# Performance work log

Measured on AMD Instinct MI355X. Metric: run time of the kernel, lower is better.

The kernel has to match this reference:

```python
import jax, jax.numpy as jnp
import numpy as np

N_HEAD = 16
LN_EPS = 1e-5     # torch LayerNorm default
ATTN_EPS = 1e-6   # fast-transformers CausalLinearAttention eps


def layer_norm(x, g, b):
    mu = x.mean(-1, keepdims=True)
    var = ((x - mu) ** 2).mean(-1, keepdims=True)
    return (x - mu) * jax.lax.rsqrt(var + LN_EPS) * g + b


def favor(x, omega):
    # Favor/Performer softmax-kernel features.
    # x: [B,S,H,dh], omega: [dh, m/2] -> phi: [B,S,H,m] with m = 2*(dh//2) = dh
    dh = x.shape[-1]
    m = 2 * omega.shape[-1]
    xs = x * (dh ** -0.25)  # x * sqrt(softmax_temp), softmax_temp = 1/sqrt(dh)
    u = jnp.einsum('bshd,dm->bshm', xs, omega)
    h = 0.5 * jnp.sum(xs * xs, axis=-1, keepdims=True)  # ||x||^2 / 2
    return jnp.concatenate([jnp.exp(u - h), jnp.exp(-u - h)], axis=-1) * (m ** -0.5)


def causal_linear_attention(q, k, v):
    # q,k: [B,S,H,M] feature-mapped; v: [B,S,H,Dv]
    # out[i] = (phiQ_i @ sum_{j<=i} phiK_j v_j^T) / (phiQ_i . sum_{j<=i} phiK_j)
    B, S, H, M = q.shape
    Dv = v.shape[-1]
    qT = jnp.moveaxis(q, 1, 0)  # [S,B,H,M]
    kT = jnp.moveaxis(k, 1, 0)
    vT = jnp.moveaxis(v, 1, 0)  # [S,B,H,Dv]
    S0 = jnp.zeros((B, H, M, Dv), q.dtype)
    z0 = jnp.zeros((B, H, M), q.dtype)

    def step(carry, qkv):
        Sst, zst = carry
        qi, ki, vi = qkv
        Sst = Sst + ki[..., :, None] * vi[..., None, :]  # [B,H,M,Dv]
        zst = zst + ki                                   # [B,H,M]
        num = jnp.einsum('bhm,bhmd->bhd', qi, Sst)
        den = jnp.einsum('bhm,bhm->bh', qi, zst) + ATTN_EPS
        return (Sst, zst), num / den[..., None]

    _, out = jax.lax.scan(step, (S0, z0), (qT, kT, vT))
    return jnp.moveaxis(out, 0, 1)  # [B,S,H,Dv]


def forward(x, Wq, bq, Wk, bk, Wv, bv, Wo, bo, omega,
            ln1_g, ln1_b, ln2_g, ln2_b, W1, bf1, W2, bf2):
    L = Wq.shape[0]
    B, S, D = x.shape
    dh = D // N_HEAD
    out = x
    for l in range(L):  # fixed small layer count
        q = (out @ Wq[l] + bq[l]).reshape(B, S, N_HEAD, dh)
        k = (out @ Wk[l] + bk[l]).reshape(B, S, N_HEAD, dh)
        v = (out @ Wv[l] + bv[l]).reshape(B, S, N_HEAD, dh)
        Qf = favor(q, omega[l])
        Kf = favor(k, omega[l])
        a = causal_linear_attention(Qf, Kf, v).reshape(B, S, D)
        a = a @ Wo[l] + bo[l]
        h = layer_norm(out + a, ln1_g[l], ln1_b[l])          # norm1 (post-norm)
        y = jax.nn.relu(h @ W1[l] + bf1[l]) @ W2[l] + bf2[l]  # FFN
        out = layer_norm(h + y, ln2_g[l], ln2_b[l])          # norm2
    return out


def setup_inputs() -> dict:
    key = jax.random.key(0)
    L, B, S, D, DFF = 3, 2, 1024, 1024, 4096
    dh = D // N_HEAD
    ks = jax.random.split(key, 8)
    g = lambda k, shape: jax.random.normal(k, shape, jnp.float32) * 0.02
    return {
        'x': jax.random.normal(ks[0], (B, S, D), jnp.float32),
        'Wq': g(ks[1], (L, D, D)), 'bq': jnp.zeros((L, D), jnp.float32),
        'Wk': g(ks[2], (L, D, D)), 'bk': jnp.zeros((L, D), jnp.float32),
        'Wv': g(ks[3], (L, D, D)), 'bv': jnp.zeros((L, D), jnp.float32),
        'Wo': g(ks[4], (L, D, D)), 'bo': jnp.zeros((L, D), jnp.float32),
        'omega': jax.random.normal(ks[5], (L, dh, dh // 2), jnp.float32),
        'ln1_g': jnp.ones((L, D), jnp.float32), 'ln1_b': jnp.zeros((L, D), jnp.float32),
        'ln2_g': jnp.ones((L, D), jnp.float32), 'ln2_b': jnp.zeros((L, D), jnp.float32),
        'W1': g(ks[6], (L, D, DFF)), 'bf1': jnp.zeros((L, DFF), jnp.float32),
        'W2': g(ks[7], (L, DFF, D)), 'bf2': jnp.zeros((L, D), jnp.float32),
    }


def reference(x, Wq, bq, Wk, bk, Wv, bv, Wo, bo, omega,
              ln1_g, ln1_b, ln2_g, ln2_b, W1, bf1, W2, bf2):
    return forward(x, Wq, bq, Wk, bk, Wv, bv, Wo, bo, omega,
                   ln1_g, ln1_b, ln2_g, ln2_b, W1, bf1, W2, bf2)
```

## Files before the change

### kernel.cpp

```cpp
#include <hip/hip_runtime.h>

typedef unsigned int u32;
typedef unsigned short u16;
typedef unsigned long long u64;

#define LN_EPS 1e-5f
#define ATTN_EPS 1e-6f

typedef __bf16 bf16x8 __attribute__((ext_vector_type(8)));
typedef short shortx8 __attribute__((ext_vector_type(8)));
typedef float fx4 __attribute__((ext_vector_type(4)));

__device__ __forceinline__ u16 f2bf(float f){
  union{float f; u32 u;} x; x.f = f;
  u32 r = 0x7fffu + ((x.u>>16)&1u);
  return (u16)((x.u + r)>>16);
}
__device__ __forceinline__ float bf2f(u16 u){
  union{u32 u; float f;} x; x.u = ((u32)u)<<16; return x.f;
}
__device__ __forceinline__ bf16x8 ldfrag(const u16* p){
  return __builtin_bit_cast(bf16x8, *(const shortx8*)p);
}

__device__ __forceinline__ void async16(const void* g, void* l){
  typedef const __attribute__((address_space(1))) void gas_t;
  typedef __attribute__((address_space(3))) void las_t;
  __builtin_amdgcn_global_load_lds((gas_t*)(u64)g, (las_t*)(u32)(u64)l, 16, 0, 0);
}

__global__ void detect_kernel(const u16* __restrict__ ln1g, int* __restrict__ flag){
  if (threadIdx.x == 0 && blockIdx.x == 0)
    *flag = (ln1g[0] == 0x3F80u) ? 1 : 0;
}

__global__ __launch_bounds__(256) void cvt_small(
    const void* p0, const void* p1, const void* p2, const void* p3,
    const void* p4, const void* p5, const void* p6, const void* p7,
    const void* p8, const void* p9, const void* p10,
    float* __restrict__ out, const int* __restrict__ flagp)
{
  int i = blockIdx.x*256 + threadIdx.x;
  if (i >= 46080) return;
  const void* src; int off;
  if      (i < 3072)  { src=p0;  off=i; }
  else if (i < 6144)  { src=p1;  off=i-3072; }
  else if (i < 9216)  { src=p2;  off=i-6144; }
  else if (i < 12288) { src=p3;  off=i-9216; }
  else if (i < 18432) { src=p4;  off=i-12288; }
  else if (i < 21504) { src=p5;  off=i-18432; }
  else if (i < 24576) { src=p6;  off=i-21504; }
  else if (i < 27648) { src=p7;  off=i-24576; }
  else if (i < 30720) { src=p8;  off=i-27648; }
  else if (i < 43008) { src=p9;  off=i-30720; }
  else                { src=p10; off=i-43008; }
  float v;
  if (*flagp){ union{u32 u; float f;} x; x.u = ((u32)((const u16*)src)[off])<<16; v = x.f; }
  else v = ((const float*)src)[off];
  out[i] = v;
}

__global__ __launch_bounds__(256) void cvt_x(const void* __restrict__ in, float* __restrict__ out,
                                             u16* __restrict__ outbf, int n, const int* __restrict__ flagp){
  int i = blockIdx.x*256 + threadIdx.x;
  if (i >= n) return;
  float v;
  if (*flagp){ union{u32 u; float f;} x; x.u = ((u32)((const u16*)in)[i])<<16; v = x.f; }
  else v = ((const float*)in)[i];
  out[i] = v;
  outbf[i] = f2bf(v);
}

__global__ __launch_bounds__(256) void transpose_cvt(
    const void* __restrict__ W, size_t eoff, u16* __restrict__ Wt,
    int K, int N, const int* __restrict__ flagp)
{
  __shared__ float s[32][33];
  const int bx = blockIdx.x, by = blockIdx.y;
  const int tid = threadIdx.x;
  const int c = tid & 31, r = tid >> 5;
  const int isbf = *flagp;
#pragma unroll
  for (int i = 0; i < 4; ++i){
    int k = by*32 + r + i*8, n = bx*32 + c;
    size_t idx = eoff + (size_t)k*N + n;
    float v;
    if (isbf){ union{u32 u; float f;} x; x.u = ((u32)((const u16*)W)[idx])<<16; v = x.f; }
    else v = ((const float*)W)[idx];
    s[r + i*8][c] = v;
  }
  __syncthreads();
#pragma unroll
  for (int i = 0; i < 4; ++i){
    int n = bx*32 + r + i*8, k = by*32 + c;
    Wt[(size_t)n*K + k] = f2bf(s[c][r + i*8]);
  }
}

__global__ __launch_bounds__(256) void transpose_cvt4(
    const void* __restrict__ W0, const void* __restrict__ W1,
    const void* __restrict__ W2, const void* __restrict__ W3,
    size_t eoff, u16* __restrict__ Wt, size_t wtz,
    int K, int N, const int* __restrict__ flagp)
{
  __shared__ float s[32][33];
  const int z = blockIdx.z;
  const void* W = (z==0)?W0:((z==1)?W1:((z==2)?W2:W3));
  Wt += (size_t)z * wtz;
  const int bx = blockIdx.x, by = blockIdx.y;
  const int tid = threadIdx.x;
  const int c = tid & 31, r = tid >> 5;
  const int isbf = *flagp;
#pragma unroll
  for (int i = 0; i < 4; ++i){
    int k = by*32 + r + i*8, n = bx*32 + c;
    size_t idx = eoff + (size_t)k*N + n;
    float v;
    if (isbf){ union{u32 u; float f;} x; x.u = ((u32)((const u16*)W)[idx])<<16; v = x.f; }
    else v = ((const float*)W)[idx];
    s[r + i*8][c] = v;
  }
  __syncthreads();
#pragma unroll
  for (int i = 0; i < 4; ++i){
    int n = bx*32 + r + i*8, k = by*32 + c;
    Wt[(size_t)n*K + k] = f2bf(s[c][r + i*8]);
  }
}

__global__ __launch_bounds__(512, 1) void mfma_gemm(
    const u16* __restrict__ A, const u16* __restrict__ W,
    const float* __restrict__ bias,
    float* __restrict__ C, u16* __restrict__ Cbf,
    int N, int Kst, int kstep_z, int klen,
    size_t wz, size_t cz, int bz, int bias_all, int relu)
{
  __shared__ u16 As[3][128*32];
  __shared__ u16 Bs[3][128*32];
  const int z = blockIdx.z;
  W    += (size_t)z * wz;
  bias += (size_t)z * bz;
  if (C) C += (size_t)z * cz;
  const int kbeg = z * kstep_z;
  const int tid = threadIdx.x;
  const int lane = tid & 63, wid = tid >> 6;

  int bx = blockIdx.x, by = blockIdx.y;
  {
    const int gx = gridDim.x, gy = gridDim.y;
    if (((gx & 3) == 0) && ((gy & 1) == 0)) {
      const int cw = gx >> 2, ch = gy >> 1;
      if (((cw & (cw-1)) == 0) && ((ch & (ch-1)) == 0)) {
        const int o = by*gx + bx;
        const int xcd = o & 7, k = o >> 3;
        const int lgw = 31 - __clz(cw);
        bx = (xcd & 3)*cw + (k & (cw-1));
        by = (xcd >> 2)*ch + (k >> lgw);
      }
    }
  }
  const int row0 = by * 128, col0 = bx * 128;

  const int ar = tid >> 2, ae = (tid & 3) << 3;
  const u16* gA0 = A + (size_t)(row0 + ar)*Kst + kbeg + ae;
  const u16* gB0 = W + (size_t)(col0 + ar)*Kst + kbeg + ae;

  const int iters = klen >> 5;
#pragma unroll
  for (int s = 0; s < 2; ++s){
    const int ko = s*32;
    async16(gA0 + ko, &As[s][tid*8]);
    async16(gB0 + ko, &Bs[s][tid*8]);
  }

  const int quad = lane >> 4, l16 = lane & 15;
  const int wr = (wid >> 2) * 64, wc = (wid & 3) * 32;
  fx4 acc[4][2] = {};

  for (int it = 0; it < iters; ++it){
    const int cur = it % 3;
    __builtin_amdgcn_s_waitcnt(0x0F72);
    __builtin_amdgcn_s_barrier();
    {
      const int nx   = (it + 2 < iters) ? (it + 2) : (iters - 1);
      const int nbuf = (it + 2) % 3;
      const int ko = nx*32;
      async16(gA0 + ko, &As[nbuf][tid*8]);
      async16(gB0 + ko, &Bs[nbuf][tid*8]);
    }
    bf16x8 af[4], bfr[2];
#pragma unroll
    for (int t = 0; t < 4; ++t)
      af[t] = ldfrag(&As[cur][(wr + t*16 + l16)*32 + quad*8]);
#pragma unroll
    for (int u = 0; u < 2; ++u)
      bfr[u] = ldfrag(&Bs[cur][(wc + u*16 + l16)*32 + quad*8]);
#pragma unroll
    for (int t = 0; t < 4; ++t)
#pragma unroll
      for (int u = 0; u < 2; ++u)
        acc[t][u] = __builtin_amdgcn_mfma_f32_16x16x32_bf16(af[t], bfr[u], acc[t][u], 0, 0, 0);
  }
  __builtin_amdgcn_s_waitcnt(0x0F70);

  const int r0 = quad * 4;
#pragma unroll
  for (int u = 0; u < 2; ++u){
    const int col = col0 + wc + u*16 + l16;
    const float bv = (bias_all || z == 0) ? bias[col] : 0.f;
#pragma unroll
    for (int t = 0; t < 4; ++t){
      const int rowb = row0 + wr + t*16 + r0;
#pragma unroll
      for (int r = 0; r < 4; ++r){
        float v = acc[t][u][r] + bv;
        if (relu) v = fmaxf(v, 0.f);
        if (C)   C[(size_t)(rowb + r)*N + col] = v;
        if (Cbf) Cbf[(size_t)(rowb + r)*N + col] = f2bf(v);
      }
    }
  }
}

__global__ __launch_bounds__(256) void favor_kernel(
    float* __restrict__ Q, float* __restrict__ Kp, const float* __restrict__ omega,
    u16* __restrict__ Qb, u16* __restrict__ Kb)
{
  __shared__ float sh[4][64];
  __shared__ float sho[64][32];
  int tid = threadIdx.x;
  for (int i = tid; i < 2048; i += 256)
    sho[i>>5][i&31] = omega[i];
  int wv = tid >> 6, lane = tid & 63;
  int th = blockIdx.x*4 + wv;
  size_t base = (size_t)(th >> 4) * 1024 + (size_t)(th & 15) * 64;
  int jm = lane & 31;
  float sgn = (lane < 32) ? 1.f : -1.f;
  for (int w = 0; w < 2; ++w){
    float* p = w ? Kp : Q;
    float xs = p[base + lane] * 0.35355339059327373f;
    __syncthreads();
    sh[wv][lane] = xs;
    __syncthreads();
    float u = 0.f, hh = 0.f;
#pragma unroll
    for (int d = 0; d < 64; ++d){
      float xv = sh[wv][d];
      u  = fmaf(xv, sho[d][jm], u);
      hh = fmaf(xv, xv, hh);
    }
    float phi = expf(sgn*u - 0.5f*hh) * 0.125f;
    if (w) p[base + lane] = phi;
    (w ? Kb : Qb)[base + lane] = f2bf(phi);
  }
}

__global__ __launch_bounds__(256) void chunk_kv(
    const float* __restrict__ Kf, const float* __restrict__ V,
    float* __restrict__ KV, float* __restrict__ Ksum)
{
  __shared__ float Ks[64][64];
  __shared__ float Vs[64][64];
  int blk = blockIdx.x;
  int c = blk & 15, h = (blk >> 4) & 15, b = blk >> 8;
  int tid = threadIdx.x;
  for (int i = tid; i < 1024; i += 256){
    int j = i >> 4, m4 = (i & 15) << 2;
    size_t src = ((size_t)(b*1024 + c*64 + j)*16 + h)*64 + m4;
    *(float4*)&Ks[j][m4] = *(const float4*)&Kf[src];
    *(float4*)&Vs[j][m4] = *(const float4*)&V[src];
  }
  __syncthreads();
  int m = tid & 63, dg = tid >> 6;
  float acc[16] = {0.f};
  for (int j = 0; j < 64; ++j){
    float kv = Ks[j][m];
#pragma unroll
    for (int di = 0; di < 16; ++di)
      acc[di] = fmaf(Vs[j][dg*16+di], kv, acc[di]);
  }
  size_t outb = (size_t)blk * 4096;
#pragma unroll
  for (int di = 0; di < 16; ++di)
    KV[outb + (size_t)(dg*16+di)*64 + m] = acc[di];
  if (tid < 64){
    float s = 0.f;
    for (int j = 0; j < 64; ++j) s += Ks[j][tid];
    Ksum[(size_t)blk*64 + tid] = s;
  }
}

__global__ __launch_bounds__(256) void chunk_scan(float* __restrict__ KV, float* __restrict__ Ksum)
{
  int blk = blockIdx.x;
  int bh = blk >> 4, ec = blk & 15;
  int e = ec*256 + threadIdx.x;
  size_t base = (size_t)bh * 65536 + e;
  float run = 0.f;
  for (int c = 0; c < 16; ++c){
    size_t idx = base + (size_t)c*4096;
    float t = KV[idx]; KV[idx] = run; run += t;
  }
  if (ec == 0 && threadIdx.x < 64){
    size_t kb = (size_t)bh * 1024 + threadIdx.x;
    float rz = 0.f;
    for (int c = 0; c < 16; ++c){
      size_t idx = kb + c*64;
      float t = Ksum[idx]; Ksum[idx] = rz; rz += t;
    }
  }
}

__global__ __launch_bounds__(256) void attn_kernel(
    const u16* __restrict__ Qbf, const u16* __restrict__ Kbf,
    const float* __restrict__ V, const float* __restrict__ KVt,
    const float* __restrict__ Ksum, u16* __restrict__ Outbf)
{
  __shared__ u16 Qs[64][72];
  __shared__ u16 Ks[64][72];
  __shared__ u16 Ss[64][72];
  __shared__ u16 Vt[64][72];
  __shared__ u16 Pt[64][72];
  __shared__ float Vrow[64][68];
  __shared__ float densum[64];

  const int blk = blockIdx.x;
  const int c = blk & 15, h = (blk >> 4) & 15, b = blk >> 8;
  const int tid = threadIdx.x;
  const int lane = tid & 63, w = tid >> 6;
  const int quad = lane >> 4, l16 = lane & 15;
  const int t0 = b*1024 + c*64;

  {
    const int r = tid >> 2, q4 = (tid & 3) << 4;
    size_t g = (size_t)(t0 + r)*1024 + h*64 + q4;
    *(uint4*)&Qs[r][q4]   = *(const uint4*)(Qbf + g);
    *(uint4*)&Qs[r][q4+8] = *(const uint4*)(Qbf + g + 8);
    *(uint4*)&Ks[r][q4]   = *(const uint4*)(Kbf + g);
    *(uint4*)&Ks[r][q4+8] = *(const uint4*)(Kbf + g + 8);
    const float* vg = V + g;
    *(float4*)&Vrow[r][q4+0]  = *(const float4*)(vg+0);
    *(float4*)&Vrow[r][q4+4]  = *(const float4*)(vg+4);
    *(float4*)&Vrow[r][q4+8]  = *(const float4*)(vg+8);
    *(float4*)&Vrow[r][q4+12] = *(const float4*)(vg+12);
    const float* pg = KVt + (size_t)blk*4096 + r*64 + q4;
    u16 tmp[16];
#pragma unroll
    for (int j = 0; j < 16; ++j) tmp[j] = f2bf(pg[j]);
    *(uint4*)&Pt[r][q4]   = *(uint4*)&tmp[0];
    *(uint4*)&Pt[r][q4+8] = *(uint4*)&tmp[8];
  }
  __syncthreads();
  {
    const int d = tid >> 2, j16 = (tid & 3) << 4;
    u16 tmp[16];
#pragma unroll
    for (int j = 0; j < 16; ++j) tmp[j] = f2bf(Vrow[j16+j][d]);
    *(uint4*)&Vt[d][j16]   = *(uint4*)&tmp[0];
    *(uint4*)&Vt[d][j16+8] = *(uint4*)&tmp[8];
  }

  const int iw0 = w*16;
  bf16x8 aq0 = ldfrag(&Qs[iw0+l16][quad*8]);
  bf16x8 aq1 = ldfrag(&Qs[iw0+l16][32+quad*8]);
  fx4 sacc[4];
#pragma unroll
  for (int u = 0; u < 4; ++u){
    sacc[u] = (fx4){0.f,0.f,0.f,0.f};
    bf16x8 b0 = ldfrag(&Ks[u*16+l16][quad*8]);
    bf16x8 b1 = ldfrag(&Ks[u*16+l16][32+quad*8]);
    sacc[u] = __builtin_amdgcn_mfma_f32_16x16x32_bf16(aq0, b0, sacc[u], 0, 0, 0);
    sacc[u] = __builtin_amdgcn_mfma_f32_16x16x32_bf16(aq1, b1, sacc[u], 0, 0, 0);
  }
  float rs[4] = {0.f,0.f,0.f,0.f};
#pragma unroll
  for (int u = 0; u < 4; ++u){
    const int jl = u*16 + l16;
#pragma unroll
    for (int r = 0; r < 4; ++r){
      const int il = iw0 + quad*4 + r;
      float v = (jl <= il) ? sacc[u][r] : 0.f;
      rs[r] += v;
      Ss[il][jl] = f2bf(v);
    }
  }
#pragma unroll
  for (int off = 1; off < 16; off <<= 1){
#pragma unroll
    for (int r = 0; r < 4; ++r) rs[r] += __shfl_xor(rs[r], off);
  }
  if (l16 == 0){
#pragma unroll
    for (int r = 0; r < 4; ++r) densum[iw0 + quad*4 + r] = rs[r];
  }
  __syncthreads();

  {
    const int row = iw0 + l16;
    const float* zp = Ksum + (size_t)blk*64;
    float dp = 0.f;
#pragma unroll
    for (int m = 0; m < 16; ++m){
      const int mm = quad*16 + m;
      dp = fmaf(bf2f(Qs[row][mm]), zp[mm], dp);
    }
    dp += __shfl_xor(dp, 16);
    dp += __shfl_xor(dp, 32);
    if (quad == 0) densum[row] = densum[row] + dp + ATTN_EPS;
  }
  __syncthreads();

  bf16x8 as0 = ldfrag(&Ss[iw0+l16][quad*8]);
  bf16x8 as1 = ldfrag(&Ss[iw0+l16][32+quad*8]);
  fx4 oacc[4];
#pragma unroll
  for (int u = 0; u < 4; ++u){
    const int d0 = u*16;
    oacc[u] = (fx4){0.f,0.f,0.f,0.f};
    oacc[u] = __builtin_amdgcn_mfma_f32_16x16x32_bf16(as0, ldfrag(&Vt[d0+l16][quad*8]),    oacc[u], 0,0,0);
    oacc[u] = __builtin_amdgcn_mfma_f32_16x16x32_bf16(as1, ldfrag(&Vt[d0+l16][32+quad*8]), oacc[u], 0,0,0);
    oacc[u] = __builtin_amdgcn_mfma_f32_16x16x32_bf16(aq0, ldfrag(&Pt[d0+l16][quad*8]),    oacc[u], 0,0,0);
    oacc[u] = __builtin_amdgcn_mfma_f32_16x16x32_bf16(aq1, ldfrag(&Pt[d0+l16][32+quad*8]), oacc[u], 0,0,0);
  }
#pragma unroll
  for (int u = 0; u < 4; ++u){
    const int d = u*16 + l16;
#pragma unroll
    for (int r = 0; r < 4; ++r){
      const int il = iw0 + quad*4 + r;
      const float o = oacc[u][r] / densum[il];
      Outbf[(size_t)(t0 + il)*1024 + h*64 + d] = f2bf(o);
    }
  }
}

__global__ __launch_bounds__(256) void resid_ln(
    const float* __restrict__ X, const float* __restrict__ Y0, const float* __restrict__ Y1,
    const float* __restrict__ g, const float* __restrict__ b,
    float* __restrict__ Dst, u16* __restrict__ DstBf,
    void* __restrict__ OutPtr, const int* __restrict__ flagp)
{
  __shared__ float rs[4], rss[4];
  int row = blockIdx.x, tid = threadIdx.x;
  int lane = tid & 63, wv = tid >> 6;
  size_t base = (size_t)row * 1024;
  int c = tid << 2;
  float4 xv = *(const float4*)&X[base + c];
  float4 y0 = *(const float4*)&Y0[base + c];
  float4 y1 = *(const float4*)&Y1[base + c];
  float v0 = xv.x+y0.x+y1.x, v1 = xv.y+y0.y+y1.y, v2 = xv.z+y0.z+y1.z, v3 = xv.w+y0.w+y1.w;
  float s = v0+v1+v2+v3;
  float ss = v0*v0+v1*v1+v2*v2+v3*v3;
  for (int off = 32; off; off >>= 1){
    s  += __shfl_down(s, off);
    ss += __shfl_down(ss, off);
  }
  if (lane == 0){ rs[wv] = s; rss[wv] = ss; }
  __syncthreads();
  float S  = rs[0]+rs[1]+rs[2]+rs[3];
  float SS = rss[0]+rss[1]+rss[2]+rss[3];
  float mu = S * (1.f/1024.f);
  float var = SS * (1.f/1024.f) - mu*mu;
  float rinv = rsqrtf(var + LN_EPS);
  float4 gv = *(const float4*)(g + c);
  float4 bb = *(const float4*)(b + c);
  float o0 = (v0-mu)*rinv*gv.x + bb.x;
  float o1 = (v1-mu)*rinv*gv.y + bb.y;
  float o2 = (v2-mu)*rinv*gv.z + bb.z;
  float o3 = (v3-mu)*rinv*gv.w + bb.w;
  *(float4*)&Dst[base + c] = make_float4(o0,o1,o2,o3);
  uint2 ob;
  ob.x = (u32)f2bf(o0) | ((u32)f2bf(o1) << 16);
  ob.y = (u32)f2bf(o2) | ((u32)f2bf(o3) << 16);
  *(uint2*)(DstBf + base + c) = ob;
  if (OutPtr){
    if (*flagp){
      *(uint2*)((u16*)OutPtr + base + c) = ob;
    } else {
      *(float4*)((float*)OutPtr + base + c) = make_float4(o0,o1,o2,o3);
    }
  }
}

extern "C" void kernel_launch(void* const* d_in, const int* in_sizes, int n_in,
                              void* d_out, int out_size, void* d_ws, size_t ws_size,
                              hipStream_t stream)
{
  (void)in_sizes; (void)n_in; (void)out_size; (void)ws_size;

  float* ws   = (float*)d_ws;
  float* bufA = ws;
  float* bufQ = bufA + 2097152;
  float* bufK = bufQ + 2097152;
  float* bufV = bufK + 2097152;
  float* KV   = bufV + 2097152;
  float* Ks   = KV   + 2097152;
  float* smallP = Ks + 32768;
  float* pend = smallP + 46080;
  int* flag = (int*)pend;
  u16* abf  = (u16*)(pend + 4);
  u16* hbf  = abf  + 2097152;
  u16* t1bf = hbf  + 2097152;
  u16* fbf  = t1bf + 2097152;
  u16* Wt   = fbf  + 8388608;
  u16* qpbf = Wt   + 4194304;
  u16* kpbf = qpbf + 2097152;

  float* bqF  = smallP + 0;
  float* boF  = smallP + 9216;
  float* omF  = smallP + 12288;
  float* l1gF = smallP + 18432;
  float* l1bF = smallP + 21504;
  float* l2gF = smallP + 24576;
  float* l2bF = smallP + 27648;
  float* bf1F = smallP + 30720;
  float* bf2F = smallP + 43008;

  detect_kernel<<<1, 64, 0, stream>>>((const u16*)d_in[10], flag);
  cvt_small<<<180, 256, 0, stream>>>(d_in[2], d_in[4], d_in[6], d_in[8], d_in[9],
                                     d_in[10], d_in[11], d_in[12], d_in[13],
                                     d_in[15], d_in[17], smallP, flag);
  cvt_x<<<8192, 256, 0, stream>>>(d_in[0], bufA, abf, 2097152, flag);

  dim3 tQKVO(32, 32, 4);
  dim3 tF1(128, 32);
  dim3 tF2(32, 128);
  dim3 gQKV(8, 16, 3);
  dim3 gO(8, 16, 2);
  dim3 gF1(32, 16, 1);
  dim3 gF2(8, 16, 2);

  for (int l = 0; l < 3; ++l){
    size_t offD = (size_t)l * 1048576;
    size_t offF = (size_t)l * 4194304;

    transpose_cvt4<<<tQKVO, 256, 0, stream>>>(d_in[1], d_in[3], d_in[5], d_in[7],
                                              offD, Wt, 1048576, 1024, 1024, flag);

    mfma_gemm<<<gQKV, 512, 0, stream>>>(abf, Wt, bqF + l*1024, bufQ, (u16*)nullptr,
                                        1024, 1024, 0, 1024,
                                        1048576, 2097152, 3072, 1, 0);
    favor_kernel<<<8192, 256, 0, stream>>>(bufQ, bufK, omF + l*2048, qpbf, kpbf);
    chunk_kv<<<512, 256, 0, stream>>>(bufK, bufV, KV, Ks);
    chunk_scan<<<512, 256, 0, stream>>>(KV, Ks);
    attn_kernel<<<512, 256, 0, stream>>>(qpbf, kpbf, bufV, KV, Ks, t1bf);

    mfma_gemm<<<gO, 512, 0, stream>>>(t1bf, Wt + 3145728, boF + l*1024, bufQ, (u16*)nullptr,
                                      1024, 1024, 512, 512,
                                      0, 4194304, 0, 0, 0);
    resid_ln<<<2048, 256, 0, stream>>>(bufA, bufQ, bufV, l1gF + l*1024, l1bF + l*1024,
                                       bufK, hbf, nullptr, flag);

    transpose_cvt<<<tF1, 256, 0, stream>>>(d_in[14], offF, Wt, 1024, 4096, flag);
    mfma_gemm<<<gF1, 512, 0, stream>>>(hbf, Wt, bf1F + l*4096, (float*)nullptr, fbf,
                                       4096, 1024, 0, 1024,
                                       0, 0, 0, 1, 1);

    transpose_cvt<<<tF2, 256, 0, stream>>>(d_in[16], offF, Wt, 4096, 1024, flag);
    mfma_gemm<<<gF2, 512, 0, stream>>>(fbf, Wt, bf2F + l*1024, bufQ, (u16*)nullptr,
                                       1024, 4096, 2048, 2048,
                                       0, 4194304, 0, 0, 0);

    resid_ln<<<2048, 256, 0, stream>>>(bufK, bufQ, bufV, l2gF + l*1024, l2bF + l*1024,
                                       bufA, abf, (l == 2) ? d_out : nullptr, flag);
  }
}
```

Measured before the change: 776.9 us.

## Hoist all weight transposes out of layer loop and shrink GEMM tiles

All layers' weights are now transposed and converted to bf16 up front in batched launches, so the per-layer transpose kernels disappear and their launches serialize less. The GEMM kernel moves from 512 threads with 128x128 tiles to 256 threads with 128x64 tiles, which doubles the number of workgroups. FFN2 split-K goes from 2 to 4 partial sums, and resid_ln is extended to add four partials. In exchange the workspace grows substantially to hold every layer's transposed weights, and the extra split-K partial buffers add memory traffic.

```diff
diff --git a/kernel.cpp b/kernel.cpp
--- a/kernel.cpp
+++ b/kernel.cpp
@@ -71,11 +71,13 @@
   outbf[i] = f2bf(v);
 }
 
-__global__ __launch_bounds__(256) void transpose_cvt(
-    const void* __restrict__ W, size_t eoff, u16* __restrict__ Wt,
-    int K, int N, const int* __restrict__ flagp)
+__global__ __launch_bounds__(256) void transpose_cvtL(
+    const void* __restrict__ W, u16* __restrict__ Wt,
+    int K, int N, size_t zsrc, size_t zdst, const int* __restrict__ flagp)
 {
   __shared__ float s[32][33];
+  const size_t eoff = (size_t)blockIdx.z * zsrc;
+  Wt += (size_t)blockIdx.z * zdst;
   const int bx = blockIdx.x, by = blockIdx.y;
   const int tid = threadIdx.x;
   const int c = tid & 31, r = tid >> 5;
@@ -97,16 +99,16 @@
   }
 }
 
-__global__ __launch_bounds__(256) void transpose_cvt4(
+__global__ __launch_bounds__(256) void transpose_cvtQ(
     const void* __restrict__ W0, const void* __restrict__ W1,
     const void* __restrict__ W2, const void* __restrict__ W3,
-    size_t eoff, u16* __restrict__ Wt, size_t wtz,
-    int K, int N, const int* __restrict__ flagp)
+    u16* __restrict__ Wt, const int* __restrict__ flagp)
 {
   __shared__ float s[32][33];
-  const int z = blockIdx.z;
-  const void* W = (z==0)?W0:((z==1)?W1:((z==2)?W2:W3));
-  Wt += (size_t)z * wtz;
+  const int z = blockIdx.z, l = z >> 2, m = z & 3;
+  const void* W = (m==0)?W0:((m==1)?W1:((m==2)?W2:W3));
+  const size_t eoff = (size_t)l * 1048576;
+  Wt += (size_t)z * 1048576;
   const int bx = blockIdx.x, by = blockIdx.y;
   const int tid = threadIdx.x;
   const int c = tid & 31, r = tid >> 5;
@@ -114,7 +116,7 @@
 #pragma unroll
   for (int i = 0; i < 4; ++i){
     int k = by*32 + r + i*8, n = bx*32 + c;
-    size_t idx = eoff + (size_t)k*N + n;
+    size_t idx = eoff + (size_t)k*1024 + n;
     float v;
     if (isbf){ union{u32 u; float f;} x; x.u = ((u32)((const u16*)W)[idx])<<16; v = x.f; }
     else v = ((const float*)W)[idx];
@@ -124,11 +126,11 @@
 #pragma unroll
   for (int i = 0; i < 4; ++i){
     int n = bx*32 + r + i*8, k = by*32 + c;
-    Wt[(size_t)n*K + k] = f2bf(s[c][r + i*8]);
-  }
-}
-
-__global__ __launch_bounds__(512, 1) void mfma_gemm(
+    Wt[(size_t)n*1024 + k] = f2bf(s[c][r + i*8]);
+  }
+}
+
+__global__ __launch_bounds__(256, 1) void mfma_gemm(
     const u16* __restrict__ A, const u16* __restrict__ W,
     const float* __restrict__ bias,
     float* __restrict__ C, u16* __restrict__ Cbf,
@@ -136,7 +138,7 @@
     size_t wz, size_t cz, int bz, int bias_all, int relu)
 {
   __shared__ u16 As[3][128*32];
-  __shared__ u16 Bs[3][128*32];
+  __shared__ u16 Bs[3][64*32];
   const int z = blockIdx.z;
   W    += (size_t)z * wz;
   bias += (size_t)z * bz;
@@ -159,10 +161,11 @@
       }
     }
   }
-  const int row0 = by * 128, col0 = bx * 128;
+  const int row0 = by * 128, col0 = bx * 64;
 
   const int ar = tid >> 2, ae = (tid & 3) << 3;
   const u16* gA0 = A + (size_t)(row0 + ar)*Kst + kbeg + ae;
+  const u16* gA1 = A + (size_t)(row0 + 64 + ar)*Kst + kbeg + ae;
   const u16* gB0 = W + (size_t)(col0 + ar)*Kst + kbeg + ae;
 
   const int iters = klen >> 5;
@@ -170,22 +173,24 @@
   for (int s = 0; s < 2; ++s){
     const int ko = s*32;
     async16(gA0 + ko, &As[s][tid*8]);
+    async16(gA1 + ko, &As[s][2048 + tid*8]);
     async16(gB0 + ko, &Bs[s][tid*8]);
   }
 
   const int quad = lane >> 4, l16 = lane & 15;
-  const int wr = (wid >> 2) * 64, wc = (wid & 3) * 32;
+  const int wr = (wid >> 1) * 64, wc = (wid & 1) * 32;
   fx4 acc[4][2] = {};
 
   for (int it = 0; it < iters; ++it){
     const int cur = it % 3;
-    __builtin_amdgcn_s_waitcnt(0x0F72);
+    __builtin_amdgcn_s_waitcnt(0x0F73);
     __builtin_amdgcn_s_barrier();
     {
       const int nx   = (it + 2 < iters) ? (it + 2) : (iters - 1);
       const int nbuf = (it + 2) % 3;
       const int ko = nx*32;
       async16(gA0 + ko, &As[nbuf][tid*8]);
+      async16(gA1 + ko, &As[nbuf][2048 + tid*8]);
       async16(gB0 + ko, &Bs[nbuf][tid*8]);
     }
     bf16x8 af[4], bfr[2];
@@ -436,6 +441,7 @@
 
 __global__ __launch_bounds__(256) void resid_ln(
     const float* __restrict__ X, const float* __restrict__ Y0, const float* __restrict__ Y1,
+    const float* __restrict__ Y2, const float* __restrict__ Y3,
     const float* __restrict__ g, const float* __restrict__ b,
     float* __restrict__ Dst, u16* __restrict__ DstBf,
     void* __restrict__ OutPtr, const int* __restrict__ flagp)
@@ -449,6 +455,11 @@
   float4 y0 = *(const float4*)&Y0[base + c];
   float4 y1 = *(const float4*)&Y1[base + c];
   float v0 = xv.x+y0.x+y1.x, v1 = xv.y+y0.y+y1.y, v2 = xv.z+y0.z+y1.z, v3 = xv.w+y0.w+y1.w;
+  if (Y2){
+    float4 y2 = *(const float4*)&Y2[base + c];
+    float4 y3 = *(const float4*)&Y3[base + c];
+    v0 += y2.x + y3.x; v1 += y2.y + y3.y; v2 += y2.z + y3.z; v3 += y2.w + y3.w;
+  }
   float s = v0+v1+v2+v3;
   float ss = v0*v0+v1*v1+v2*v2+v3*v3;
   for (int off = 32; off; off >>= 1){
@@ -489,12 +500,13 @@
   (void)in_sizes; (void)n_in; (void)out_size; (void)ws_size;
 
   float* ws   = (float*)d_ws;
-  float* bufA = ws;
-  float* bufQ = bufA + 2097152;
-  float* bufK = bufQ + 2097152;
-  float* bufV = bufK + 2097152;
-  float* KV   = bufV + 2097152;
-  float* Ks   = KV   + 2097152;
+  float* R    = ws;
+  float* P0   = R  + 2097152;
+  float* P1   = P0 + 2097152;
+  float* P2   = P1 + 2097152;
+  float* P3   = P2 + 2097152;
+  float* KVb  = P3 + 2097152;
+  float* Ks   = KVb + 2097152;
   float* smallP = Ks + 32768;
   float* pend = smallP + 46080;
   int* flag = (int*)pend;
@@ -502,9 +514,11 @@
   u16* hbf  = abf  + 2097152;
   u16* t1bf = hbf  + 2097152;
   u16* fbf  = t1bf + 2097152;
-  u16* Wt   = fbf  + 8388608;
-  u16* qpbf = Wt   + 4194304;
+  u16* qpbf = fbf  + 8388608;
   u16* kpbf = qpbf + 2097152;
+  u16* WtQ  = kpbf + 2097152;
+  u16* WtF1 = WtQ  + 12582912;
+  u16* WtF2 = WtF1 + 12582912;
 
   float* bqF  = smallP + 0;
   float* boF  = smallP + 9216;
@@ -520,48 +534,48 @@
   cvt_small<<<180, 256, 0, stream>>>(d_in[2], d_in[4], d_in[6], d_in[8], d_in[9],
                                      d_in[10], d_in[11], d_in[12], d_in[13],
                                      d_in[15], d_in[17], smallP, flag);
-  cvt_x<<<8192, 256, 0, stream>>>(d_in[0], bufA, abf, 2097152, flag);
-
-  dim3 tQKVO(32, 32, 4);
-  dim3 tF1(128, 32);
-  dim3 tF2(32, 128);
-  dim3 gQKV(8, 16, 3);
-  dim3 gO(8, 16, 2);
-  dim3 gF1(32, 16, 1);
-  dim3 gF2(8, 16, 2);
+  cvt_x<<<8192, 256, 0, stream>>>(d_in[0], R, abf, 2097152, flag);
+
+  transpose_cvtQ<<<dim3(32, 32, 12), 256, 0, stream>>>(d_in[1], d_in[3], d_in[5], d_in[7],
+                                                       WtQ, flag);
+  transpose_cvtL<<<dim3(128, 32, 3), 256, 0, stream>>>(d_in[14], WtF1, 1024, 4096,
+                                                       4194304, 4194304, flag);
+  transpose_cvtL<<<dim3(32, 128, 3), 256, 0, stream>>>(d_in[16], WtF2, 4096, 1024,
+                                                       4194304, 4194304, flag);
+
+  dim3 gQKV(16, 16, 3);
+  dim3 gO(16, 16, 2);
+  dim3 gF1(64, 16, 1);
+  dim3 gF2(16, 16, 4);
 
   for (int l = 0; l < 3; ++l){
-    size_t offD = (size_t)l * 1048576;
-    size_t offF = (size_t)l * 4194304;
-
-    transpose_cvt4<<<tQKVO, 256, 0, stream>>>(d_in[1], d_in[3], d_in[5], d_in[7],
-                                              offD, Wt, 1048576, 1024, 1024, flag);
-
-    mfma_gemm<<<gQKV, 512, 0, stream>>>(abf, Wt, bqF + l*1024, bufQ, (u16*)nullptr,
+    const size_t wQ = (size_t)l * 4194304;
+
+    mfma_gemm<<<gQKV, 256, 0, stream>>>(abf, WtQ + wQ, bqF + l*1024, P0, (u16*)nullptr,
                                         1024, 1024, 0, 1024,
                                         1048576, 2097152, 3072, 1, 0);
-    favor_kernel<<<8192, 256, 0, stream>>>(bufQ, bufK, omF + l*2048, qpbf, kpbf);
-    chunk_kv<<<512, 256, 0, stream>>>(bufK, bufV, KV, Ks);
-    chunk_scan<<<512, 256, 0, stream>>>(KV, Ks);
-    attn_kernel<<<512, 256, 0, stream>>>(qpbf, kpbf, bufV, KV, Ks, t1bf);
-
-    mfma_gemm<<<gO, 512, 0, stream>>>(t1bf, Wt + 3145728, boF + l*1024, bufQ, (u16*)nullptr,
+    favor_kernel<<<8192, 256, 0, stream>>>(P0, P1, omF + l*2048, qpbf, kpbf);
+    chunk_kv<<<512, 256, 0, stream>>>(P1, P2, KVb, Ks);
+    chunk_scan<<<512, 256, 0, stream>>>(KVb, Ks);
+    attn_kernel<<<512, 256, 0, stream>>>(qpbf, kpbf, P2, KVb, Ks, t1bf);
+
+    mfma_gemm<<<gO, 256, 0, stream>>>(t1bf, WtQ + wQ + 3145728, boF + l*1024, P0, (u16*)nullptr,
                                       1024, 1024, 512, 512,
-                                      0, 4194304, 0, 0, 0);
-    resid_ln<<<2048, 256, 0, stream>>>(bufA, bufQ, bufV, l1gF + l*1024, l1bF + l*1024,
-                                       bufK, hbf, nullptr, flag);
-
-    transpose_cvt<<<tF1, 256, 0, stream>>>(d_in[14], offF, Wt, 1024, 4096, flag);
-    mfma_gemm<<<gF1, 512, 0, stream>>>(hbf, Wt, bf1F + l*4096, (float*)nullptr, fbf,
+                                      0, 2097152, 0, 0, 0);
+    resid_ln<<<2048, 256, 0, stream>>>(R, P0, P1, nullptr, nullptr,
+                                       l1gF + l*1024, l1bF + l*1024,
+                                       KVb, hbf, nullptr, flag);
+
+    mfma_gemm<<<gF1, 256, 0, stream>>>(hbf, WtF1 + wQ, bf1F + l*4096, (float*)nullptr, fbf,
                                        4096, 1024, 0, 1024,
                                        0, 0, 0, 1, 1);
 
-    transpose_cvt<<<tF2, 256, 0, stream>>>(d_in[16], offF, Wt, 4096, 1024, flag);
-    mfma_gemm<<<gF2, 512, 0, stream>>>(fbf, Wt, bf2F + l*1024, bufQ, (u16*)nullptr,
-                                       1024, 4096, 2048, 2048,
-                                       0, 4194304, 0, 0, 0);
-
-    resid_ln<<<2048, 256, 0, stream>>>(bufK, bufQ, bufV, l2gF + l*1024, l2bF + l*1024,
-                                       bufA, abf, (l == 2) ? d_out : nullptr, flag);
-  }
-}
+    mfma_gemm<<<gF2, 256, 0, stream>>>(fbf, WtF2 + wQ, bf2F + l*1024, P0, (u16*)nullptr,
+                                       1024, 4096, 1024, 1024,
+                                       0, 2097152, 0, 0, 0);
+
+    resid_ln<<<2048, 256, 0, stream>>>(KVb, P0, P1, P2, P3,
+                                       l2gF + l*1024, l2bF + l*1024,
+                                       R, abf, (l == 2) ? d_out : nullptr, flag);
+  }
+}
```

Result: slower. 857.2 us (+10.3%).
